# Optimization experiments

Measured on AMD Instinct MI355X. Metric: run time of the kernel, lower is better.

## Reference

```python
import jax, jax.numpy as jnp
import numpy as np

B, T = 64, 524288          # batch, samples (~32.8 s @ 16 kHz)
D = 16                      # downsample_factor for the envelope follower
SR = 16000
EPS = 1e-7                  # avoids log10(0) in level detection


def _time_const(ms):
    # exp(-log10(9) / (sr * ms * 1e-3 * downsample_factor)), as in __init__
    return float(np.exp(-np.log10(9.0) / (SR * ms * 0.001 * D)))


def setup_inputs() -> dict:
    key = jax.random.key(0)
    audio = jax.random.normal(key, (B, T), dtype=jnp.float32) * 0.5
    return {
        "audio": audio,
        "threshold": jnp.float32(-30.0),               # dB
        "ratio": jnp.float32(4.0),
        "makeup": jnp.float32(6.0),                    # dB
        "attack_time": jnp.float32(_time_const(5.0)),
        "release_time": jnp.float32(_time_const(100.0)),
    }


def reference(audio, threshold, ratio, makeup, attack_time, release_time):
    # --- level detection in dB ---
    x_db = 20.0 * jnp.log10(jnp.abs(audio) + EPS)            # [B, T]
    # --- time-averaged downsampling by D (frame mean) ---
    x_db_ds = x_db.reshape(B, T // D, D).mean(axis=-1)       # [B, T//D]
    # --- static gain computer ---
    y_db = jnp.where(x_db_ds > threshold,
                     threshold + (x_db_ds - threshold) / ratio,
                     x_db_ds)
    g = y_db - x_db_ds                                       # desired gain in dB (<= 0)

    # --- attack/release envelope follower: sample-recurrent one-pole IIR ---
    def step(prev, g_t):
        alpha = jnp.where(g_t < prev, attack_time, release_time)
        new = alpha * prev + (1.0 - alpha) * g_t
        return new, new

    _, g_s = jax.lax.scan(step, jnp.zeros((B,), audio.dtype), g.T)  # [T//D, B]

    # --- upsample smoothed gain back to audio rate and apply with makeup ---
    gain = jnp.repeat(g_s.T, D, axis=1)                      # [B, T]
    return audio * jnp.power(jnp.float32(10.0), (gain + makeup) / 20.0)
```

## Files before the change

kernel.cpp:

```cpp
#include <hip/hip_runtime.h>

#define B_DIM 64
#define T_DIM 524288
#define D_FAC 16
#define LBLK 64
#define NB 512
#define NBLK_TOT 32768
#define CSTR 72
#define PF 16
#define EPSV 1e-7f
#define BIGC 1e30f

#define DB_PER_LOG2 6.0205999132796239f
#define L2TEN_OVER20 0.16609640474436813f

__device__ __forceinline__ float sum_log2_4(float4 x) {
  return __log2f(fabsf(x.x) + EPSV) + __log2f(fabsf(x.y) + EPSV) +
         __log2f(fabsf(x.z) + EPSV) + __log2f(fabsf(x.w) + EPSV);
}

template <int CTRL, int RM>
__device__ __forceinline__ float fmin_dpp_step(float v) {
  int vi = __float_as_int(v);
  int sh = __builtin_amdgcn_update_dpp(vi, vi, CTRL, RM, 0xf, false);
  return fminf(v, __int_as_float(sh));
}

__global__ __launch_bounds__(256) void k1_compose(
    const float* __restrict__ audio, const float* __restrict__ p_thr,
    const float* __restrict__ p_ratio, const float* __restrict__ p_att,
    const float* __restrict__ p_rel, float* __restrict__ consts) {
  __shared__ float cab[4][128];
  const int tid = threadIdx.x;
  const int lane = tid & 63;
  const int w = tid >> 6;
  const int gblk = blockIdx.x * 4 + w;
  const int row = gblk >> 9;
  const int b = gblk & (NB - 1);
  const float thr = p_thr[0];
  const float A = p_att[0], R = p_rel[0];
  const float oneA = 1.f - A, oneR = 1.f - R;
  const float gslope = (1.f / p_ratio[0]) - 1.f;

  const size_t sbase = (size_t)row * T_DIM + (size_t)(b * LBLK + lane) * D_FAC;
  const float4* ap = (const float4*)(audio + sbase);
  float s = sum_log2_4(ap[0]) + sum_log2_4(ap[1]) + sum_log2_4(ap[2]) +
            sum_log2_4(ap[3]);
  float xdb = s * (DB_PER_LOG2 / 16.f);
  float g = fminf(0.f, (xdb - thr) * gslope);

  cab[w][2 * lane] = oneA * g;
  cab[w][2 * lane + 1] = oneR * g;

  const float2* cp = (const float2*)cab[w];
  float c = (lane == 0) ? 0.f : BIGC;
  float c64 = BIGC;
#pragma unroll
  for (int t = 0; t < LBLK; ++t) {
    float2 cc = cp[t];
    float prev = __int_as_float(__builtin_amdgcn_update_dpp(
        __float_as_int(BIGC), __float_as_int(c), 0x138 , 0xf,
        0xf, false));
    c64 = fminf(fmaf(A, c, cc.x), fmaf(R, c64, cc.y));
    c = fminf(fmaf(A, prev, cc.x), fmaf(R, c, cc.y));
  }
  float* outp = consts + (size_t)gblk * CSTR;
  outp[lane] = c;
  if (lane == 63) {
#pragma unroll
    for (int j = 0; j < 8; ++j) outp[64 + j] = c64;
  }
}

__global__ __launch_bounds__(64) void k2_scan(const float* __restrict__ consts,
                                              float* __restrict__ states,
                                              const float* __restrict__ p_att,
                                              const float* __restrict__ p_rel) {
  const int r = blockIdx.x;
  const int lane = threadIdx.x;
  const float A = p_att[0], R = p_rel[0];
  const int cls0 = (lane < 8) ? 8 * lane : 64;
  float s0 = 1.f;
  for (int i = 0; i < 64; ++i) s0 *= (i < cls0) ? A : R;
  const float rAR = A / R;
  const float sl0 = s0, sl1 = sl0 * rAR, sl2 = sl1 * rAR, sl3 = sl2 * rAR,
              sl4 = sl3 * rAR, sl5 = sl4 * rAR, sl6 = sl5 * rAR,
              sl7 = sl6 * rAR;

  const float* base = consts + (size_t)r * NB * CSTR;
  float* st = states + r * NB;
  const int loff = (lane < 8) ? 8 * lane : 64;

  float4 qa[PF], qb[PF];
#pragma unroll
  for (int u = 0; u < PF; ++u) {
    qa[u] = *(const float4*)(base + u * CSTR + loff);
    qb[u] = *(const float4*)(base + u * CSTR + loff + 4);
  }

  float p = 0.f;
  for (int j = 0; j < 8; ++j) {
    float sj = 0.f;
    for (int k = 0; k < 4; ++k) {
#pragma unroll
      for (int u = 0; u < PF; ++u) {
        const int b = j * 64 + k * PF + u;
        const int i = k * PF + u;
        float f0 = fmaf(sl0, p, qa[u].x);
        float f1 = fmaf(sl1, p, qa[u].y);
        float f2 = fmaf(sl2, p, qa[u].z);
        float f3 = fmaf(sl3, p, qa[u].w);
        float f4 = fmaf(sl4, p, qb[u].x);
        float f5 = fmaf(sl5, p, qb[u].y);
        float f6 = fmaf(sl6, p, qb[u].z);
        float f7 = fmaf(sl7, p, qb[u].w);
        float m = fminf(fminf(fminf(f0, f1), f2),
                        fminf(fminf(fminf(f3, f4), f5), fminf(f6, f7)));
        m = fmin_dpp_step<0x111, 0xf>(m);
        m = fmin_dpp_step<0x112, 0xf>(m);
        m = fmin_dpp_step<0x114, 0xf>(m);
        m = fmin_dpp_step<0x111, 0xf>(m);
        sj = (lane == i) ? p : sj;
        p = __int_as_float(__builtin_amdgcn_readlane(__float_as_int(m), 8));
        qa[u] = *(const float4*)(base + (b + PF) * CSTR + loff);
        qb[u] = *(const float4*)(base + (b + PF) * CSTR + loff + 4);
      }
    }
    st[j * 64 + lane] = sj;
  }
}

__global__ __launch_bounds__(256) void k3_apply(
    const float* __restrict__ audio, const float* __restrict__ states,
    const float* __restrict__ p_thr, const float* __restrict__ p_ratio,
    const float* __restrict__ p_makeup, const float* __restrict__ p_att,
    const float* __restrict__ p_rel, float* __restrict__ out) {
  const int tid = threadIdx.x;
  const int lane = tid & 63;
  const int w = tid >> 6;
  const int gblk = blockIdx.x * 4 + w;
  const int row = gblk >> 9;
  const int b = gblk & (NB - 1);
  const float thr = p_thr[0], ratio = p_ratio[0], mk = p_makeup[0];
  const float A = p_att[0], R = p_rel[0];
  const float oneA = 1.f - A, oneR = 1.f - R;
  const float gslope = (1.f / ratio) - 1.f;

  const size_t sbase = (size_t)row * T_DIM + (size_t)(b * LBLK + lane) * D_FAC;
  const float4* ap = (const float4*)(audio + sbase);
  float4 x0 = ap[0], x1 = ap[1], x2 = ap[2], x3 = ap[3];
  float s = sum_log2_4(x0) + sum_log2_4(x1) + sum_log2_4(x2) + sum_log2_4(x3);
  float xdb = s * (DB_PER_LOG2 / 16.f);
  float g = fminf(0.f, (xdb - thr) * gslope);

  float p = states[gblk];
  float m = 0.f;
  int gi = __float_as_int(g);
#pragma unroll
  for (int t = 0; t < LBLK; ++t) {
    float gt = __int_as_float(__builtin_amdgcn_readlane(gi, t));
    p = fminf(fmaf(A, p, oneA * gt), fmaf(R, p, oneR * gt));
    m = (lane == t) ? p : m;
  }
  float mult = exp2f((m + mk) * L2TEN_OVER20);
  float4* op = (float4*)(out + sbase);
  float4 y0, y1, y2, y3;
  y0.x = x0.x * mult; y0.y = x0.y * mult; y0.z = x0.z * mult; y0.w = x0.w * mult;
  y1.x = x1.x * mult; y1.y = x1.y * mult; y1.z = x1.z * mult; y1.w = x1.w * mult;
  y2.x = x2.x * mult; y2.y = x2.y * mult; y2.z = x2.z * mult; y2.w = x2.w * mult;
  y3.x = x3.x * mult; y3.y = x3.y * mult; y3.z = x3.z * mult; y3.w = x3.w * mult;
  op[0] = y0; op[1] = y1; op[2] = y2; op[3] = y3;
}

extern "C" void kernel_launch(void* const* d_in, const int* in_sizes, int n_in,
                              void* d_out, int out_size, void* d_ws,
                              size_t ws_size, hipStream_t stream) {
  const float* audio = (const float*)d_in[0];
  const float* thr = (const float*)d_in[1];
  const float* ratio = (const float*)d_in[2];
  const float* makeup = (const float*)d_in[3];
  const float* att = (const float*)d_in[4];
  const float* rel = (const float*)d_in[5];
  float* out = (float*)d_out;

  const size_t CONSTS_BYTES = (size_t)NBLK_TOT * CSTR * sizeof(float);
  const size_t PAD_BYTES = (size_t)PF * CSTR * sizeof(float);
  const size_t STATES_BYTES = (size_t)NBLK_TOT * sizeof(float);

  float* consts;
  float* states;
  if (ws_size >= CONSTS_BYTES + PAD_BYTES + STATES_BYTES) {
    consts = (float*)d_ws;
    states = (float*)((char*)d_ws + CONSTS_BYTES + PAD_BYTES);
  } else {
    consts = (float*)d_out;
    states = (float*)d_ws;
  }

  hipLaunchKernelGGL(k1_compose, dim3(8192), dim3(256), 0, stream, audio, thr,
                     ratio, att, rel, consts);
  hipLaunchKernelGGL(k2_scan, dim3(64), dim3(64), 0, stream, consts, states,
                     att, rel);
  hipLaunchKernelGGL(k3_apply, dim3(8192), dim3(256), 0, stream, audio, states,
                     thr, ratio, makeup, att, rel, out);
}
```

Measured before the change: 140.8 us.

## Double per-wave block length to 128 frames, halving serial scan steps

Each wave now composes the envelope recurrence over 128 downsampled frames instead of 64, with each lane handling two frames and the piecewise-min function described by 129 classes. The per-row serial scan in k2 therefore walks 256 blocks instead of 512, cutting the latency-bound sequential chain in half. In exchange, k1 and k3 each run a 128-step serial loop per wave with more registers, and k2 has to reduce 16 lanes and handle an extra class per step.

```diff
diff --git a/kernel.cpp b/kernel.cpp
--- a/kernel.cpp
+++ b/kernel.cpp
@@ -3,11 +3,13 @@
 #define B_DIM 64
 #define T_DIM 524288
 #define D_FAC 16
-#define LBLK 64
-#define NB 512
-#define NBLK_TOT 32768
-#define CSTR 72
+#define LBLK 128
+#define NB 256
+#define NBLK_TOT 16384
+#define NCLS 129
+#define CSTR 132
 #define PF 16
+#define PADBLK 16
 #define EPSV 1e-7f
 #define BIGC 1e30f
 
@@ -30,46 +32,53 @@
     const float* __restrict__ audio, const float* __restrict__ p_thr,
     const float* __restrict__ p_ratio, const float* __restrict__ p_att,
     const float* __restrict__ p_rel, float* __restrict__ consts) {
-  __shared__ float cab[4][128];
+  __shared__ float cab[4][256];
   const int tid = threadIdx.x;
   const int lane = tid & 63;
   const int w = tid >> 6;
   const int gblk = blockIdx.x * 4 + w;
-  const int row = gblk >> 9;
+  const int row = gblk >> 8;
   const int b = gblk & (NB - 1);
   const float thr = p_thr[0];
   const float A = p_att[0], R = p_rel[0];
   const float oneA = 1.f - A, oneR = 1.f - R;
   const float gslope = (1.f / p_ratio[0]) - 1.f;
 
-  const size_t sbase = (size_t)row * T_DIM + (size_t)(b * LBLK + lane) * D_FAC;
-  const float4* ap = (const float4*)(audio + sbase);
-  float s = sum_log2_4(ap[0]) + sum_log2_4(ap[1]) + sum_log2_4(ap[2]) +
-            sum_log2_4(ap[3]);
-  float xdb = s * (DB_PER_LOG2 / 16.f);
-  float g = fminf(0.f, (xdb - thr) * gslope);
-
-  cab[w][2 * lane] = oneA * g;
-  cab[w][2 * lane + 1] = oneR * g;
+  const size_t base0 =
+      (size_t)row * T_DIM + (size_t)(b * LBLK + lane) * D_FAC;
+  const float4* ap0 = (const float4*)(audio + base0);
+  const float4* ap1 = (const float4*)(audio + base0 + 64 * D_FAC);
+  float4 x0 = ap0[0], x1 = ap0[1], x2 = ap0[2], x3 = ap0[3];
+  float4 x4 = ap1[0], x5 = ap1[1], x6 = ap1[2], x7 = ap1[3];
+  float s0 = sum_log2_4(x0) + sum_log2_4(x1) + sum_log2_4(x2) + sum_log2_4(x3);
+  float s1 = sum_log2_4(x4) + sum_log2_4(x5) + sum_log2_4(x6) + sum_log2_4(x7);
+  float g0 = fminf(0.f, (s0 * (DB_PER_LOG2 / 16.f) - thr) * gslope);
+  float g1 = fminf(0.f, (s1 * (DB_PER_LOG2 / 16.f) - thr) * gslope);
+
+  cab[w][2 * lane] = oneA * g0;
+  cab[w][2 * lane + 1] = oneR * g0;
+  cab[w][128 + 2 * lane] = oneA * g1;
+  cab[w][128 + 2 * lane + 1] = oneR * g1;
 
   const float2* cp = (const float2*)cab[w];
-  float c = (lane == 0) ? 0.f : BIGC;
-  float c64 = BIGC;
+  float c0 = (lane == 0) ? 0.f : BIGC;
+  float c1 = BIGC;
+  float c128 = BIGC;
 #pragma unroll
   for (int t = 0; t < LBLK; ++t) {
     float2 cc = cp[t];
     float prev = __int_as_float(__builtin_amdgcn_update_dpp(
-        __float_as_int(BIGC), __float_as_int(c), 0x138 , 0xf,
+        __float_as_int(BIGC), __float_as_int(c1), 0x138 , 0xf,
         0xf, false));
-    c64 = fminf(fmaf(A, c, cc.x), fmaf(R, c64, cc.y));
-    c = fminf(fmaf(A, prev, cc.x), fmaf(R, c, cc.y));
+    float n128 = fminf(fmaf(A, c1, cc.x), fmaf(R, c128, cc.y));
+    float n1 = fminf(fmaf(A, c0, cc.x), fmaf(R, c1, cc.y));
+    float n0 = fminf(fmaf(A, prev, cc.x), fmaf(R, c0, cc.y));
+    c128 = n128; c1 = n1; c0 = n0;
   }
   float* outp = consts + (size_t)gblk * CSTR;
-  outp[lane] = c;
-  if (lane == 63) {
-#pragma unroll
-    for (int j = 0; j < 8; ++j) outp[64 + j] = c64;
-  }
+  float2 pr; pr.x = c0; pr.y = c1;
+  *(float2*)(outp + 2 * lane) = pr;
+  if (lane == 63) outp[128] = c128;
 }
 
 __global__ __launch_bounds__(64) void k2_scan(const float* __restrict__ consts,
@@ -79,32 +88,37 @@
   const int r = blockIdx.x;
   const int lane = threadIdx.x;
   const float A = p_att[0], R = p_rel[0];
-  const int cls0 = (lane < 8) ? 8 * lane : 64;
+  const int cls0 = (lane < 15) ? 8 * lane : 120;
   float s0 = 1.f;
-  for (int i = 0; i < 64; ++i) s0 *= (i < cls0) ? A : R;
+  for (int i = 0; i < 128; ++i) s0 *= (i < cls0) ? A : R;
   const float rAR = A / R;
   const float sl0 = s0, sl1 = sl0 * rAR, sl2 = sl1 * rAR, sl3 = sl2 * rAR,
               sl4 = sl3 * rAR, sl5 = sl4 * rAR, sl6 = sl5 * rAR,
               sl7 = sl6 * rAR;
+  const float sl8 = sl7 * rAR;
+  const int loff = (lane < 15) ? 8 * lane : 120;
+  const bool is15 = (lane == 15);
 
   const float* base = consts + (size_t)r * NB * CSTR;
   float* st = states + r * NB;
-  const int loff = (lane < 8) ? 8 * lane : 64;
 
   float4 qa[PF], qb[PF];
+  float qc[PF];
 #pragma unroll
   for (int u = 0; u < PF; ++u) {
     qa[u] = *(const float4*)(base + u * CSTR + loff);
     qb[u] = *(const float4*)(base + u * CSTR + loff + 4);
+    float t = base[u * CSTR + 128];
+    qc[u] = is15 ? t : BIGC;
   }
 
   float p = 0.f;
-  for (int j = 0; j < 8; ++j) {
+  for (int j = 0; j < 4; ++j) {
     float sj = 0.f;
     for (int k = 0; k < 4; ++k) {
 #pragma unroll
       for (int u = 0; u < PF; ++u) {
-        const int b = j * 64 + k * PF + u;
+        const int b2 = j * 64 + k * PF + u;
         const int i = k * PF + u;
         float f0 = fmaf(sl0, p, qa[u].x);
         float f1 = fmaf(sl1, p, qa[u].y);
@@ -114,16 +128,19 @@
         float f5 = fmaf(sl5, p, qb[u].y);
         float f6 = fmaf(sl6, p, qb[u].z);
         float f7 = fmaf(sl7, p, qb[u].w);
-        float m = fminf(fminf(fminf(f0, f1), f2),
-                        fminf(fminf(fminf(f3, f4), f5), fminf(f6, f7)));
+        float f8 = fmaf(sl8, p, qc[u]);
+        float m = fminf(fminf(fminf(f0, f1), fminf(f2, f3)),
+                        fminf(fminf(f4, f5), fminf(fminf(f6, f7), f8)));
         m = fmin_dpp_step<0x111, 0xf>(m);
         m = fmin_dpp_step<0x112, 0xf>(m);
         m = fmin_dpp_step<0x114, 0xf>(m);
-        m = fmin_dpp_step<0x111, 0xf>(m);
+        m = fmin_dpp_step<0x118, 0xf>(m);
         sj = (lane == i) ? p : sj;
-        p = __int_as_float(__builtin_amdgcn_readlane(__float_as_int(m), 8));
-        qa[u] = *(const float4*)(base + (b + PF) * CSTR + loff);
-        qb[u] = *(const float4*)(base + (b + PF) * CSTR + loff + 4);
+        p = __int_as_float(__builtin_amdgcn_readlane(__float_as_int(m), 15));
+        qa[u] = *(const float4*)(base + (b2 + PF) * CSTR + loff);
+        qb[u] = *(const float4*)(base + (b2 + PF) * CSTR + loff + 4);
+        float t2 = base[(b2 + PF) * CSTR + 128];
+        qc[u] = is15 ? t2 : BIGC;
       }
     }
     st[j * 64 + lane] = sj;
@@ -139,37 +156,52 @@
   const int lane = tid & 63;
   const int w = tid >> 6;
   const int gblk = blockIdx.x * 4 + w;
-  const int row = gblk >> 9;
+  const int row = gblk >> 8;
   const int b = gblk & (NB - 1);
   const float thr = p_thr[0], ratio = p_ratio[0], mk = p_makeup[0];
   const float A = p_att[0], R = p_rel[0];
   const float oneA = 1.f - A, oneR = 1.f - R;
   const float gslope = (1.f / ratio) - 1.f;
 
-  const size_t sbase = (size_t)row * T_DIM + (size_t)(b * LBLK + lane) * D_FAC;
-  const float4* ap = (const float4*)(audio + sbase);
-  float4 x0 = ap[0], x1 = ap[1], x2 = ap[2], x3 = ap[3];
-  float s = sum_log2_4(x0) + sum_log2_4(x1) + sum_log2_4(x2) + sum_log2_4(x3);
-  float xdb = s * (DB_PER_LOG2 / 16.f);
-  float g = fminf(0.f, (xdb - thr) * gslope);
+  const size_t base0 =
+      (size_t)row * T_DIM + (size_t)(b * LBLK + lane) * D_FAC;
+  const float4* ap0 = (const float4*)(audio + base0);
+  const float4* ap1 = (const float4*)(audio + base0 + 64 * D_FAC);
+  float4 x0 = ap0[0], x1 = ap0[1], x2 = ap0[2], x3 = ap0[3];
+  float4 x4 = ap1[0], x5 = ap1[1], x6 = ap1[2], x7 = ap1[3];
+  float s0 = sum_log2_4(x0) + sum_log2_4(x1) + sum_log2_4(x2) + sum_log2_4(x3);
+  float s1 = sum_log2_4(x4) + sum_log2_4(x5) + sum_log2_4(x6) + sum_log2_4(x7);
+  float g0 = fminf(0.f, (s0 * (DB_PER_LOG2 / 16.f) - thr) * gslope);
+  float g1 = fminf(0.f, (s1 * (DB_PER_LOG2 / 16.f) - thr) * gslope);
 
   float p = states[gblk];
-  float m = 0.f;
-  int gi = __float_as_int(g);
-#pragma unroll
-  for (int t = 0; t < LBLK; ++t) {
-    float gt = __int_as_float(__builtin_amdgcn_readlane(gi, t));
+  float m0 = 0.f, m1 = 0.f;
+  const int gi0 = __float_as_int(g0), gi1 = __float_as_int(g1);
+#pragma unroll
+  for (int t = 0; t < 64; ++t) {
+    float gt = __int_as_float(__builtin_amdgcn_readlane(gi0, t));
     p = fminf(fmaf(A, p, oneA * gt), fmaf(R, p, oneR * gt));
-    m = (lane == t) ? p : m;
-  }
-  float mult = exp2f((m + mk) * L2TEN_OVER20);
-  float4* op = (float4*)(out + sbase);
-  float4 y0, y1, y2, y3;
-  y0.x = x0.x * mult; y0.y = x0.y * mult; y0.z = x0.z * mult; y0.w = x0.w * mult;
-  y1.x = x1.x * mult; y1.y = x1.y * mult; y1.z = x1.z * mult; y1.w = x1.w * mult;
-  y2.x = x2.x * mult; y2.y = x2.y * mult; y2.z = x2.z * mult; y2.w = x2.w * mult;
-  y3.x = x3.x * mult; y3.y = x3.y * mult; y3.z = x3.z * mult; y3.w = x3.w * mult;
-  op[0] = y0; op[1] = y1; op[2] = y2; op[3] = y3;
+    m0 = (lane == t) ? p : m0;
+  }
+#pragma unroll
+  for (int t = 0; t < 64; ++t) {
+    float gt = __int_as_float(__builtin_amdgcn_readlane(gi1, t));
+    p = fminf(fmaf(A, p, oneA * gt), fmaf(R, p, oneR * gt));
+    m1 = (lane == t) ? p : m1;
+  }
+  float mult0 = exp2f((m0 + mk) * L2TEN_OVER20);
+  float mult1 = exp2f((m1 + mk) * L2TEN_OVER20);
+  float4* op0 = (float4*)(out + base0);
+  float4* op1 = (float4*)(out + base0 + 64 * D_FAC);
+  float4 y;
+  y.x = x0.x * mult0; y.y = x0.y * mult0; y.z = x0.z * mult0; y.w = x0.w * mult0; op0[0] = y;
+  y.x = x1.x * mult0; y.y = x1.y * mult0; y.z = x1.z * mult0; y.w = x1.w * mult0; op0[1] = y;
+  y.x = x2.x * mult0; y.y = x2.y * mult0; y.z = x2.z * mult0; y.w = x2.w * mult0; op0[2] = y;
+  y.x = x3.x * mult0; y.y = x3.y * mult0; y.z = x3.z * mult0; y.w = x3.w * mult0; op0[3] = y;
+  y.x = x4.x * mult1; y.y = x4.y * mult1; y.z = x4.z * mult1; y.w = x4.w * mult1; op1[0] = y;
+  y.x = x5.x * mult1; y.y = x5.y * mult1; y.z = x5.z * mult1; y.w = x5.w * mult1; op1[1] = y;
+  y.x = x6.x * mult1; y.y = x6.y * mult1; y.z = x6.z * mult1; y.w = x6.w * mult1; op1[2] = y;
+  y.x = x7.x * mult1; y.y = x7.y * mult1; y.z = x7.z * mult1; y.w = x7.w * mult1; op1[3] = y;
 }
 
 extern "C" void kernel_launch(void* const* d_in, const int* in_sizes, int n_in,
@@ -183,24 +215,24 @@
   const float* rel = (const float*)d_in[5];
   float* out = (float*)d_out;
 
-  const size_t CONSTS_BYTES = (size_t)NBLK_TOT * CSTR * sizeof(float);
-  const size_t PAD_BYTES = (size_t)PF * CSTR * sizeof(float);
+  const size_t CONSTS_BYTES =
+      (size_t)(NBLK_TOT + PADBLK) * CSTR * sizeof(float);
   const size_t STATES_BYTES = (size_t)NBLK_TOT * sizeof(float);
 
   float* consts;
   float* states;
-  if (ws_size >= CONSTS_BYTES + PAD_BYTES + STATES_BYTES) {
+  if (ws_size >= CONSTS_BYTES + STATES_BYTES) {
     consts = (float*)d_ws;
-    states = (float*)((char*)d_ws + CONSTS_BYTES + PAD_BYTES);
+    states = (float*)((char*)d_ws + CONSTS_BYTES);
   } else {
     consts = (float*)d_out;
     states = (float*)d_ws;
   }
 
-  hipLaunchKernelGGL(k1_compose, dim3(8192), dim3(256), 0, stream, audio, thr,
+  hipLaunchKernelGGL(k1_compose, dim3(4096), dim3(256), 0, stream, audio, thr,
                      ratio, att, rel, consts);
   hipLaunchKernelGGL(k2_scan, dim3(64), dim3(64), 0, stream, consts, states,
                      att, rel);
-  hipLaunchKernelGGL(k3_apply, dim3(8192), dim3(256), 0, stream, audio, states,
+  hipLaunchKernelGGL(k3_apply, dim3(4096), dim3(256), 0, stream, audio, states,
                      thr, ratio, makeup, att, rel, out);
 }
```

Result: slower. 165.5 us (+17.6%).
